# Performance work log

Hardware: AMD Instinct MI355X
Metric: run time of the kernel (lower is better)

## Reference

```python
import jax, jax.numpy as jnp
import numpy as np

N, DIN, DOUT, C = 4096, 64, 16, 4

def setup_inputs() -> dict:
    key = jax.random.key(0)
    k1, k2, k3, k4 = jax.random.split(key, 4)
    features = jax.random.normal(k1, (N, DIN, C), dtype=jnp.float32)
    adj = jax.random.uniform(k2, (N, N, C), dtype=jnp.float32)
    stdv = 1.0 / np.sqrt(DOUT)
    weight = jax.random.uniform(k3, (DIN, DOUT, C), dtype=jnp.float32, minval=-stdv, maxval=stdv)
    bias = jax.random.uniform(k4, (N, DOUT, C), dtype=jnp.float32, minval=-stdv, maxval=stdv)
    return {"features": features, "adj": adj, "weight": weight, "bias": bias}

def _fft_product(X, W):
    # circular convolution along the last (channel) axis via FFT
    Xf = jnp.fft.fft(X, axis=-1)
    Wf = jnp.fft.fft(W, axis=-1)
    return jnp.fft.ifft(jnp.einsum('ijk,jrk->irk', Xf, Wf), axis=-1).real

def reference(features, adj, weight, bias):
    support = _fft_product(features, weight)      # [N, DOUT, C]
    output = _fft_product(adj, support)           # [N, DOUT, C]
    return output + bias
```

## Files before the change

### kernel.cpp

```cpp
#include <hip/hip_runtime.h>

#define NN 4096
#define DIN 64
#define DOUTC 16
#define CCH 4
#define K_TOT (NN*CCH)
#define N_OUT (DOUTC*CCH)

typedef __bf16 bf16x8 __attribute__((ext_vector_type(8)));
typedef __bf16 bf16x4 __attribute__((ext_vector_type(4)));
typedef float  f32x4  __attribute__((ext_vector_type(4)));

__global__ void bias_init_kernel(const float* __restrict__ bias,
                                 float* __restrict__ out) {
    int t = blockIdx.x * blockDim.x + threadIdx.x;
    ((f32x4*)out)[t] = ((const f32x4*)bias)[t];
}

__global__ void support_kernel(const float* __restrict__ feat,
                               const float* __restrict__ wgt,
                               __bf16* __restrict__ Bt) {
    const int t  = threadIdx.x;
    const int r  = t & 15;
    const int jl = t >> 4;
    const int j  = blockIdx.x * 16 + jl;

    float a0 = 0.f, a1 = 0.f, a2 = 0.f, a3 = 0.f;
    const f32x4* f4 = (const f32x4*)(feat + (size_t)j * DIN * CCH);
    const f32x4* w4 = (const f32x4*)wgt;
    #pragma unroll 8
    for (int d = 0; d < DIN; ++d) {
        f32x4 f = f4[d];
        f32x4 w = w4[d * 16 + r];
        a0 += f[0]*w[0] + f[1]*w[3] + f[2]*w[2] + f[3]*w[1];
        a1 += f[0]*w[1] + f[1]*w[0] + f[2]*w[3] + f[3]*w[2];
        a2 += f[0]*w[2] + f[1]*w[1] + f[2]*w[0] + f[3]*w[3];
        a3 += f[0]*w[3] + f[1]*w[2] + f[2]*w[1] + f[3]*w[0];
    }
    float accs[4] = {a0, a1, a2, a3};
    #pragma unroll
    for (int cc = 0; cc < 4; ++cc) {
        #pragma unroll
        for (int cp = 0; cp < 4; ++cp) {
            int n = r * 4 + ((cc + cp) & 3);
            Bt[(size_t)n * K_TOT + j * 4 + cp] = (__bf16)accs[cc];
        }
    }
}

#define BM 64
#define BK 128
#define KCHUNKS 8
#define KSPLIT 16

__launch_bounds__(256, 4)
__global__ void gemm_kernel(const float* __restrict__ A,
                            const __bf16* __restrict__ Bt,
                            float* __restrict__ out) {
    __shared__ __align__(16) __bf16 lA[BM * BK];
    __shared__ __align__(16) __bf16 lB[N_OUT * BK];

    const int t    = threadIdx.x;
    const int wave = t >> 6;
    const int lane = t & 63;
    const int i0   = blockIdx.x * BM;
    const int kbase = blockIdx.y * (KCHUNKS * BK);

    char* lAc = (char*)lA;
    char* lBc = (char*)lB;

    f32x4 acc[4] = {};

    const int mrow = wave * 16 + (lane & 15);
    const int kgrp = lane >> 4;

    for (int c = 0; c < KCHUNKS; ++c) {
        const int k0 = kbase + c * BK;
        #pragma unroll
        for (int it = 0; it < 8; ++it) {
            int idx = it * 256 + t;
            int m   = idx >> 5;
            int c4  = idx & 31;
            f32x4 v = *(const f32x4*)(A + (size_t)(i0 + m) * K_TOT + k0 + c4 * 4);
            bf16x4 b;
            b[0] = (__bf16)v[0]; b[1] = (__bf16)v[1];
            b[2] = (__bf16)v[2]; b[3] = (__bf16)v[3];
            int byte = (m * 256 + c4 * 8) ^ ((m & 7) << 4);
            *(bf16x4*)(lAc + byte) = b;
        }
        #pragma unroll
        for (int it = 0; it < 4; ++it) {
            int idx = it * 256 + t;
            int n   = idx >> 4;
            int c8  = idx & 15;
            uint4 v = *(const uint4*)(Bt + (size_t)n * K_TOT + k0 + c8 * 8);
            int byte = (n * 256 + c8 * 16) ^ ((n & 7) << 4);
            *(uint4*)(lBc + byte) = v;
        }
        __syncthreads();

        #pragma unroll
        for (int kk = 0; kk < 4; ++kk) {
            int abyte = (mrow * 256 + kk * 64 + kgrp * 16) ^ ((mrow & 7) << 4);
            bf16x8 af = *(const bf16x8*)(lAc + abyte);
            #pragma unroll
            for (int nf = 0; nf < 4; ++nf) {
                int n = nf * 16 + (lane & 15);
                int bbyte = (n * 256 + kk * 64 + kgrp * 16) ^ ((n & 7) << 4);
                bf16x8 bf = *(const bf16x8*)(lBc + bbyte);
                acc[nf] = __builtin_amdgcn_mfma_f32_16x16x32_bf16(af, bf, acc[nf], 0, 0, 0);
            }
        }
        __syncthreads();
    }

    const int col  = lane & 15;
    const int rowg = lane >> 4;
    #pragma unroll
    for (int nf = 0; nf < 4; ++nf) {
        #pragma unroll
        for (int e = 0; e < 4; ++e) {
            int i = i0 + wave * 16 + rowg * 4 + e;
            int n = nf * 16 + col;
            atomicAdd(&out[(size_t)i * N_OUT + n], acc[nf][e]);
        }
    }
}

extern "C" void kernel_launch(void* const* d_in, const int* in_sizes, int n_in,
                              void* d_out, int out_size, void* d_ws, size_t ws_size,
                              hipStream_t stream) {
    const float* feat = (const float*)d_in[0];
    const float* adj  = (const float*)d_in[1];
    const float* wgt  = (const float*)d_in[2];
    const float* bias = (const float*)d_in[3];
    float* out = (float*)d_out;
    __bf16* Bt = (__bf16*)d_ws;

    bias_init_kernel<<<256, 256, 0, stream>>>(bias, out);
    support_kernel<<<NN / 16, 256, 0, stream>>>(feat, wgt, Bt);
    dim3 grid(NN / BM, KSPLIT);
    gemm_kernel<<<grid, 256, 0, stream>>>(adj, Bt, out);
}
```

Before: 409.5 us.

## Load GEMM operands directly from global and replace atomics with split-K reduction

New measurement: 424.3 us. 3.6% more time.

```diff
diff --git a/kernel.cpp b/kernel.cpp
--- a/kernel.cpp
+++ b/kernel.cpp
@@ -6,16 +6,12 @@
 #define CCH 4
 #define K_TOT (NN*CCH)
 #define N_OUT (DOUTC*CCH)
+#define SPLITS 16
+#define KRANGE (K_TOT/SPLITS)
 
 typedef __bf16 bf16x8 __attribute__((ext_vector_type(8)));
 typedef __bf16 bf16x4 __attribute__((ext_vector_type(4)));
 typedef float  f32x4  __attribute__((ext_vector_type(4)));
-
-__global__ void bias_init_kernel(const float* __restrict__ bias,
-                                 float* __restrict__ out) {
-    int t = blockIdx.x * blockDim.x + threadIdx.x;
-    ((f32x4*)out)[t] = ((const f32x4*)bias)[t];
-}
 
 __global__ void support_kernel(const float* __restrict__ feat,
                                const float* __restrict__ wgt,
@@ -39,92 +35,70 @@
     }
     float accs[4] = {a0, a1, a2, a3};
     #pragma unroll
-    for (int cc = 0; cc < 4; ++cc) {
+    for (int c = 0; c < 4; ++c) {
+        bf16x4 b;
+        b[0] = (__bf16)accs[c];
+        b[1] = (__bf16)accs[(c + 3) & 3];
+        b[2] = (__bf16)accs[(c + 2) & 3];
+        b[3] = (__bf16)accs[(c + 1) & 3];
+        *(bf16x4*)(Bt + (size_t)(r * 4 + c) * K_TOT + j * 4) = b;
+    }
+}
+
+__launch_bounds__(256)
+__global__ void gemm_kernel(const float* __restrict__ A,
+                            const __bf16* __restrict__ Bt,
+                            float* __restrict__ part) {
+    const int t    = threadIdx.x;
+    const int wave = t >> 6;
+    const int lane = t & 63;
+    const int row  = blockIdx.x * 64 + wave * 16 + (lane & 15);
+    const int kq   = lane >> 4;
+    const int kbase = blockIdx.y * KRANGE;
+
+    const float*  Ap = A  + (size_t)row * K_TOT + kbase + kq * 8;
+    const __bf16* Bp = Bt + (size_t)(lane & 15) * K_TOT + kbase + kq * 8;
+
+    f32x4 acc[4] = {};
+
+    #pragma unroll 2
+    for (int ks = 0; ks < KRANGE / 32; ++ks) {
+        f32x4 a0 = *(const f32x4*)(Ap + ks * 32);
+        f32x4 a1 = *(const f32x4*)(Ap + ks * 32 + 4);
+        bf16x8 af;
+        af[0] = (__bf16)a0[0]; af[1] = (__bf16)a0[1];
+        af[2] = (__bf16)a0[2]; af[3] = (__bf16)a0[3];
+        af[4] = (__bf16)a1[0]; af[5] = (__bf16)a1[1];
+        af[6] = (__bf16)a1[2]; af[7] = (__bf16)a1[3];
         #pragma unroll
-        for (int cp = 0; cp < 4; ++cp) {
-            int n = r * 4 + ((cc + cp) & 3);
-            Bt[(size_t)n * K_TOT + j * 4 + cp] = (__bf16)accs[cc];
+        for (int nf = 0; nf < 4; ++nf) {
+            bf16x8 bf = *(const bf16x8*)(Bp + (size_t)nf * 16 * K_TOT + ks * 32);
+            acc[nf] = __builtin_amdgcn_mfma_f32_16x16x32_bf16(af, bf, acc[nf], 0, 0, 0);
+        }
+    }
+
+    const int col  = lane & 15;
+    const int rowg = lane >> 4;
+    float* P = part + ((size_t)blockIdx.y * NN + blockIdx.x * 64 + wave * 16) * N_OUT;
+    #pragma unroll
+    for (int nf = 0; nf < 4; ++nf) {
+        #pragma unroll
+        for (int e = 0; e < 4; ++e) {
+            P[(rowg * 4 + e) * N_OUT + nf * 16 + col] = acc[nf][e];
         }
     }
 }
 
-#define BM 64
-#define BK 128
-#define KCHUNKS 8
-#define KSPLIT 16
-
-__launch_bounds__(256, 4)
-__global__ void gemm_kernel(const float* __restrict__ A,
-                            const __bf16* __restrict__ Bt,
-                            float* __restrict__ out) {
-    __shared__ __align__(16) __bf16 lA[BM * BK];
-    __shared__ __align__(16) __bf16 lB[N_OUT * BK];
-
-    const int t    = threadIdx.x;
-    const int wave = t >> 6;
-    const int lane = t & 63;
-    const int i0   = blockIdx.x * BM;
-    const int kbase = blockIdx.y * (KCHUNKS * BK);
-
-    char* lAc = (char*)lA;
-    char* lBc = (char*)lB;
-
-    f32x4 acc[4] = {};
-
-    const int mrow = wave * 16 + (lane & 15);
-    const int kgrp = lane >> 4;
-
-    for (int c = 0; c < KCHUNKS; ++c) {
-        const int k0 = kbase + c * BK;
-        #pragma unroll
-        for (int it = 0; it < 8; ++it) {
-            int idx = it * 256 + t;
-            int m   = idx >> 5;
-            int c4  = idx & 31;
-            f32x4 v = *(const f32x4*)(A + (size_t)(i0 + m) * K_TOT + k0 + c4 * 4);
-            bf16x4 b;
-            b[0] = (__bf16)v[0]; b[1] = (__bf16)v[1];
-            b[2] = (__bf16)v[2]; b[3] = (__bf16)v[3];
-            int byte = (m * 256 + c4 * 8) ^ ((m & 7) << 4);
-            *(bf16x4*)(lAc + byte) = b;
-        }
-        #pragma unroll
-        for (int it = 0; it < 4; ++it) {
-            int idx = it * 256 + t;
-            int n   = idx >> 4;
-            int c8  = idx & 15;
-            uint4 v = *(const uint4*)(Bt + (size_t)n * K_TOT + k0 + c8 * 8);
-            int byte = (n * 256 + c8 * 16) ^ ((n & 7) << 4);
-            *(uint4*)(lBc + byte) = v;
-        }
-        __syncthreads();
-
-        #pragma unroll
-        for (int kk = 0; kk < 4; ++kk) {
-            int abyte = (mrow * 256 + kk * 64 + kgrp * 16) ^ ((mrow & 7) << 4);
-            bf16x8 af = *(const bf16x8*)(lAc + abyte);
-            #pragma unroll
-            for (int nf = 0; nf < 4; ++nf) {
-                int n = nf * 16 + (lane & 15);
-                int bbyte = (n * 256 + kk * 64 + kgrp * 16) ^ ((n & 7) << 4);
-                bf16x8 bf = *(const bf16x8*)(lBc + bbyte);
-                acc[nf] = __builtin_amdgcn_mfma_f32_16x16x32_bf16(af, bf, acc[nf], 0, 0, 0);
-            }
-        }
-        __syncthreads();
+__global__ void reduce_kernel(const float* __restrict__ part,
+                              const float* __restrict__ bias,
+                              float* __restrict__ out) {
+    int t = blockIdx.x * blockDim.x + threadIdx.x;
+    f32x4 s = ((const f32x4*)bias)[t];
+    #pragma unroll
+    for (int sp = 0; sp < SPLITS; ++sp) {
+        s += ((const f32x4*)(part + (size_t)sp * NN * N_OUT))[t];
     }
-
-    const int col  = lane & 15;
-    const int rowg = lane >> 4;
-    #pragma unroll
-    for (int nf = 0; nf < 4; ++nf) {
-        #pragma unroll
-        for (int e = 0; e < 4; ++e) {
-            int i = i0 + wave * 16 + rowg * 4 + e;
-            int n = nf * 16 + col;
-            atomicAdd(&out[(size_t)i * N_OUT + n], acc[nf][e]);
-        }
-    }
+    ((f32x4*)out)[t] = s;
 }
 
 extern "C" void kernel_launch(void* const* d_in, const int* in_sizes, int n_in,
@@ -135,10 +109,12 @@
     const float* wgt  = (const float*)d_in[2];
     const float* bias = (const float*)d_in[3];
     float* out = (float*)d_out;
-    __bf16* Bt = (__bf16*)d_ws;
 
-    bias_init_kernel<<<256, 256, 0, stream>>>(bias, out);
+    float*  part = (float*)d_ws;
+    __bf16* Bt   = (__bf16*)((char*)d_ws + (size_t)SPLITS * NN * N_OUT * 4);
+
     support_kernel<<<NN / 16, 256, 0, stream>>>(feat, wgt, Bt);
-    dim3 grid(NN / BM, KSPLIT);
-    gemm_kernel<<<grid, 256, 0, stream>>>(adj, Bt, out);
+    dim3 grid(NN / 64, SPLITS);
+    gemm_kernel<<<grid, 256, 0, stream>>>(adj, Bt, part);
+    reduce_kernel<<<NN * N_OUT / 4 / 256, 256, 0, stream>>>(part, bias, out);
 }
```
